# Kernel tuning notes

Measured on AMD Instinct MI355X. Metric: run time of the kernel, lower is better.

Reference implementation:

```python
import jax, jax.numpy as jnp
import numpy as np

B, D = 8192, 512
MARGIN, CR_BETA, NUM_CLASSES = 0.2, 0.1, 1000


def setup_inputs() -> dict:
    key = jax.random.key(0)
    k1, k2, k3, k4 = jax.random.split(key, 4)
    return {
        "img": jax.random.normal(k1, (B, D), jnp.float32),
        "txt": jax.random.normal(k2, (B, D), jnp.float32),
        "txt_cr": jax.random.normal(k3, (B, D), jnp.float32),
        "labels": jax.random.randint(k4, (B,), 0, NUM_CLASSES),
        "auto_margin_flag": 1,
        "margin": jnp.full((B,), MARGIN, jnp.float32),  # opt.margin repeated per row
        "cr_beta": CR_BETA,
    }


def _similarity(a, b):
    # row-normalize then full cosine-similarity matrix + matched (diagonal) sims
    an = a / (jnp.linalg.norm(a, axis=1, keepdims=True) + 1e-8)
    bn = b / (jnp.linalg.norm(b, axis=1, keepdims=True) + 1e-8)
    return an @ bn.T, jnp.sum(an * bn, axis=1)


def _dir_loss(sim, labels, margin, auto_flag):
    # semi-hard negative mining per anchor row, fully vectorized.
    # Deterministic stand-in for np.random.choice: first valid negative index.
    diag = jnp.diagonal(sim)                               # sim[idx, idx]
    neg_mask = labels[None, :] != labels[:, None]          # [B,B] negatives
    loss_mat = sim - diag[:, None] + margin[:, None]       # triplet margin term
    valid = neg_mask & (loss_mat > 0) & (loss_mat < margin[:, None])
    valid = jax.lax.stop_gradient(valid)                   # mining is detached (numpy in torch)
    has_valid = jnp.any(valid, axis=1)
    if auto_flag:
        row_ok = (margin >= 0.16) & has_valid
    else:
        row_ok = has_valid
    neg_idx = jnp.argmax(valid, axis=1)                    # first valid negative
    sim_an = jnp.take_along_axis(sim, neg_idx[:, None], axis=1)[:, 0]
    per_row = jax.nn.relu(margin - diag + sim_an)
    return jnp.sum(jnp.where(row_ok, per_row, 0.0))


def _cr_loss(img, txt, txt_cr, labels, auto_flag, margin, cr_beta):
    sim, sm = _similarity(img, txt)
    sim_cr, sm_cr = _similarity(img, txt_cr)
    if auto_flag:
        lam = jnp.abs(jax.lax.stop_gradient(sm_cr)) / jnp.abs(jax.lax.stop_gradient(sm))
        lam = jnp.minimum(lam, 1.0)                        # clamp lambda_cr to <= 1
        margin_cr = (lam + 1.0) * margin / 2.0
    else:
        margin_cr = margin / 2.0
    margin_cr = jax.lax.stop_gradient(margin_cr)
    base = _dir_loss(sim, labels, margin, auto_flag) + _dir_loss(sim.T, labels, margin, auto_flag)
    cr = _dir_loss(sim_cr, labels, margin_cr, auto_flag) + _dir_loss(sim_cr.T, labels, margin_cr, auto_flag)
    return base + cr_beta * cr


def reference(img, txt, txt_cr, labels, auto_margin_flag, margin, cr_beta):
    return _cr_loss(img, txt, txt_cr, labels, bool(auto_margin_flag), margin, cr_beta)
```

## Files before the change

### kernel.cpp

```cpp
#include <hip/hip_runtime.h>
#include <climits>

#define NB 8192
#define ND 512

#define WCHUNKS 16
#define WTILES 8
#define TCHUNKS ((NB - 64) / 64)


__global__ __launch_bounds__(256) void stats_k(
        const float* __restrict__ img, const float* __restrict__ txt,
        const float* __restrict__ cr, const float* __restrict__ margin,
        const int* __restrict__ flagp,
        float* rnImg, float* rnTxt, float* rnCr,
        float* dgSim, float* dgCr, float* mgCr,
        int* negIdx, int* stragCnt, float* out) {
    int tid = threadIdx.x, bid = blockIdx.x;
    int g = bid * 256 + tid;
    if (g < 4 * NB) negIdx[g] = INT_MAX;
    if (bid == 0 && tid < 8) stragCnt[tid] = 0;
    if (bid == 0 && tid == 0) out[0] = 0.0f;

    int r = bid * 16 + (tid >> 4);
    int q = tid & 15;
    const float4* iv = (const float4*)(img + (size_t)r * ND);
    const float4* tv = (const float4*)(txt + (size_t)r * ND);
    const float4* cv = (const float4*)(cr  + (size_t)r * ND);
    float sii = 0, stt = 0, scc = 0, sit = 0, sic = 0;
    #pragma unroll
    for (int i = 0; i < 8; ++i) {
        int k = q + i * 16;
        float4 x = iv[k], y = tv[k], w = cv[k];
        sii += x.x*x.x + x.y*x.y + x.z*x.z + x.w*x.w;
        stt += y.x*y.x + y.y*y.y + y.z*y.z + y.w*y.w;
        scc += w.x*w.x + w.y*w.y + w.z*w.z + w.w*w.w;
        sit += x.x*y.x + x.y*y.y + x.z*y.z + x.w*y.w;
        sic += x.x*w.x + x.y*w.y + x.z*w.z + x.w*w.w;
    }
    #pragma unroll
    for (int off = 1; off < 16; off <<= 1) {
        sii += __shfl_xor(sii, off); stt += __shfl_xor(stt, off);
        scc += __shfl_xor(scc, off); sit += __shfl_xor(sit, off);
        sic += __shfl_xor(sic, off);
    }
    if (q == 0) {
        float rnI = 1.0f / (sqrtf(sii) + 1e-8f);
        float rnT = 1.0f / (sqrtf(stt) + 1e-8f);
        float rnC = 1.0f / (sqrtf(scc) + 1e-8f);
        float ds = sit * rnI * rnT;
        float dc = sic * rnI * rnC;
        float m  = margin[r];
        float mcr = flagp[0] ? (fminf(fabsf(dc) / fabsf(ds), 1.0f) + 1.0f) * m * 0.5f
                             : m * 0.5f;
        rnImg[r] = rnI; rnTxt[r] = rnT; rnCr[r] = rnC;
        dgSim[r] = ds;  dgCr[r]  = dc;  mgCr[r] = mcr;
    }
}

__device__ inline void pass_arrays(int z,
        const float* img, const float* txt, const float* cr,
        const float* rnImg, const float* rnTxt, const float* rnCr,
        const float* dgSim, const float* dgCr,
        const float* margin, const float* mgCr,
        const float*& A, const float*& B, const float*& rnA, const float*& rnB,
        const float*& dgA, const float*& mgA) {
    if (z == 0)      { A = img; B = txt; rnA = rnImg; rnB = rnTxt; dgA = dgSim; mgA = margin; }
    else if (z == 1) { A = txt; B = img; rnA = rnTxt; rnB = rnImg; dgA = dgSim; mgA = margin; }
    else if (z == 2) { A = img; B = cr;  rnA = rnImg; rnB = rnCr;  dgA = dgCr;  mgA = mgCr;   }
    else             { A = cr;  B = img; rnA = rnCr;  rnB = rnImg; dgA = dgCr;  mgA = mgCr;   }
}

template <bool GATHER>
__device__ __forceinline__ void gemm32x64(
        const float* __restrict__ A, const float* __restrict__ B,
        int a0, const int* aRow, int c0,
        float (&As)[16][36], float (&Bs)[16][68],
        float (&acc)[2][4], int tid) {
    const int ty2 = (tid >> 4) * 2, tx4 = (tid & 15) * 4;
    const int lrow = tid >> 2, lk4 = (tid & 3) * 4;
    const bool doA = tid < 128;
    const int arow = GATHER ? (doA ? aRow[lrow] : 0) : (a0 + (lrow & 31));
    float4 va, vb;
    if (doA) va = *(const float4*)(A + (size_t)arow * ND + lk4);
    vb = *(const float4*)(B + (size_t)(c0 + lrow) * ND + lk4);
    for (int kc = 0; kc < ND; kc += 16) {
        __syncthreads();
        if (doA) {
            As[lk4 + 0][lrow] = va.x; As[lk4 + 1][lrow] = va.y;
            As[lk4 + 2][lrow] = va.z; As[lk4 + 3][lrow] = va.w;
        }
        Bs[lk4 + 0][lrow] = vb.x; Bs[lk4 + 1][lrow] = vb.y;
        Bs[lk4 + 2][lrow] = vb.z; Bs[lk4 + 3][lrow] = vb.w;
        if (kc + 16 < ND) {
            if (doA) va = *(const float4*)(A + (size_t)arow * ND + kc + 16 + lk4);
            vb = *(const float4*)(B + (size_t)(c0 + lrow) * ND + kc + 16 + lk4);
        }
        __syncthreads();
        #pragma unroll
        for (int k = 0; k < 16; ++k) {
            float2 av = *(const float2*)&As[k][ty2];
            float4 bv = *(const float4*)&Bs[k][tx4];
            #pragma unroll
            for (int i = 0; i < 2; ++i) {
                float ai = i ? av.y : av.x;
                acc[i][0] = fmaf(ai, bv.x, acc[i][0]);
                acc[i][1] = fmaf(ai, bv.y, acc[i][1]);
                acc[i][2] = fmaf(ai, bv.z, acc[i][2]);
                acc[i][3] = fmaf(ai, bv.w, acc[i][3]);
            }
        }
    }
}

__global__ __launch_bounds__(256) void band_k(
        const float* __restrict__ img, const float* __restrict__ txt,
        const float* __restrict__ cr, const int* __restrict__ labels,
        const int* __restrict__ flagp, const float* __restrict__ margin,
        const float* __restrict__ betap,
        const float* rnImg, const float* rnTxt, const float* rnCr,
        const float* dgSim, const float* dgCr, const float* mgCr,
        int* stragCnt, int* stragList, float* out) {
    __shared__ __align__(16) float As[16][36];
    __shared__ __align__(16) float Bs[16][68];
    __shared__ float aRn[32], aDg[32], aMg[32], colRn[64];
    __shared__ int   aLab[32], colLab[64], resIdx[32];
    __shared__ float blockAcc;

    const int tid = threadIdx.x, z = blockIdx.y, a0 = blockIdx.x * 32;
    const int flag = flagp[0];
    const float *A, *B, *rnA, *rnB, *dgA, *mgA;
    pass_arrays(z, img, txt, cr, rnImg, rnTxt, rnCr, dgSim, dgCr, margin, mgCr,
                A, B, rnA, rnB, dgA, mgA);

    if (tid < 32) {
        int a = a0 + tid;
        float mg = mgA[a];
        aRn[tid] = rnA[a]; aDg[tid] = dgA[a]; aMg[tid] = mg;
        aLab[tid] = labels[a];
        resIdx[tid] = (flag && mg < 0.16f) ? -1 : INT_MAX;
    }
    if (tid < 64) { colRn[tid] = rnB[tid]; colLab[tid] = labels[tid]; }
    if (tid == 0) blockAcc = 0.0f;
    __syncthreads();

    float acc[2][4] = {};
    gemm32x64<false>(A, B, a0, nullptr, 0, As, Bs, acc, tid);
    __syncthreads();

    const int ty2 = (tid >> 4) * 2, tx4 = (tid & 15) * 4;
    #pragma unroll
    for (int i = 0; i < 2; ++i) {
        int r = ty2 + i;
        float mgv = aMg[r];
        if (flag && mgv < 0.16f) continue;
        float dg = aDg[r], rna = aRn[r];
        int la = aLab[r];
        #pragma unroll
        for (int j = 0; j < 4; ++j) {
            int c = tx4 + j;
            if (colLab[c] == la) continue;
            float lm = acc[i][j] * rna * colRn[c] - dg + mgv;
            if (lm > 0.0f && lm < mgv) atomicMin(&resIdx[r], c);
        }
    }
    __syncthreads();

    #pragma unroll
    for (int i = 0; i < 2; ++i) {
        int r = ty2 + i;
        int w = resIdx[r];
        if (w < 0 || w == INT_MAX) continue;
        int c = w - tx4;
        if (c < 0 || c > 3) continue;
        float lm = acc[i][c] * aRn[r] * colRn[w] - aDg[r] + aMg[r];
        atomicAdd(&blockAcc, lm);
    }
    __syncthreads();

    if (tid < 32 && resIdx[tid] == INT_MAX) {
        int pos = atomicAdd(&stragCnt[z], 1);
        stragList[z * NB + pos] = a0 + tid;
    }
    if (tid == 0 && blockAcc != 0.0f) {
        float scale = (z >= 2) ? betap[0] : 1.0f;
        atomicAdd(out, blockAcc * scale);
    }
}

__global__ __launch_bounds__(256) void wina_k(
        const float* __restrict__ img, const float* __restrict__ txt,
        const float* __restrict__ cr, const int* __restrict__ labels,
        const float* __restrict__ margin,
        const float* rnImg, const float* rnTxt, const float* rnCr,
        const float* dgSim, const float* dgCr, const float* mgCr,
        const int* stragCnt, const int* stragList, int* negIdx) {
    __shared__ __align__(16) float As[16][36];
    __shared__ __align__(16) float Bs[16][68];
    __shared__ float aRn[32], aDg[32], aMg[32], colRn[64];
    __shared__ int   aId[32], aRow[32], aLab[32], colLab[64];

    const int tid = threadIdx.x, z = blockIdx.y;
    const int chunk = blockIdx.x & (WCHUNKS - 1);
    const int t     = blockIdx.x / WCHUNKS;
    const int cnt = stragCnt[z];
    if (t * 32 >= cnt) return;
    const int c0 = 64 + chunk * 64;

    const float *A, *B, *rnA, *rnB, *dgA, *mgA;
    pass_arrays(z, img, txt, cr, rnImg, rnTxt, rnCr, dgSim, dgCr, margin, mgCr,
                A, B, rnA, rnB, dgA, mgA);

    if (tid < 32) {
        int s = t * 32 + tid;
        int a = (s < cnt) ? stragList[z * NB + s] : -1;
        int ar = (a >= 0) ? a : 0;
        aId[tid] = a; aRow[tid] = ar;
        aRn[tid] = rnA[ar]; aDg[tid] = dgA[ar]; aMg[tid] = mgA[ar];
        aLab[tid] = labels[ar];
    }
    if (tid < 64) { colRn[tid] = rnB[c0 + tid]; colLab[tid] = labels[c0 + tid]; }
    __syncthreads();

    float acc[2][4] = {};
    gemm32x64<true>(A, B, 0, aRow, c0, As, Bs, acc, tid);
    __syncthreads();

    const int ty2 = (tid >> 4) * 2, tx4 = (tid & 15) * 4;
    #pragma unroll
    for (int i = 0; i < 2; ++i) {
        int r = ty2 + i;
        int a = aId[r];
        if (a < 0) continue;
        float dg = aDg[r], mgv = aMg[r], rna = aRn[r];
        int la = aLab[r];
        #pragma unroll
        for (int j = 0; j < 4; ++j) {
            int c = tx4 + j;
            if (colLab[c] == la) continue;
            float lm = acc[i][j] * rna * colRn[c] - dg + mgv;
            if (lm > 0.0f && lm < mgv) atomicMin(&negIdx[z * NB + a], c0 + c);
        }
    }
}

__device__ inline float dot8(const float4& a0, const float4& a1,
                             const float4& b0, const float4& b1) {
    return a0.x*b0.x + a0.y*b0.y + a0.z*b0.z + a0.w*b0.w
         + a1.x*b1.x + a1.y*b1.y + a1.z*b1.z + a1.w*b1.w;
}

__global__ __launch_bounds__(256) void tail_k(
        const float* __restrict__ img, const float* __restrict__ txt,
        const float* __restrict__ cr, const int* __restrict__ labels,
        const float* __restrict__ margin,
        const float* rnImg, const float* rnTxt, const float* rnCr,
        const float* dgSim, const float* dgCr, const float* mgCr,
        const int* stragCnt, const int* stragList, int* negIdx) {
    __shared__ __align__(16) float Aload[8][ND];
    __shared__ float sRn[8], sDg[8], sMg[8];
    __shared__ int   sLab[8], sAid[8];
    __shared__ float colRn_s[64];
    __shared__ int   colLab_s[64];
    __shared__ int   sSurv[256];
    __shared__ int   sNa;

    const int tid = threadIdx.x, z = blockIdx.y;
    const int c0 = 64 + blockIdx.x * 64;
    const int cnt = stragCnt[z];
    if (cnt == 0) return;

    const float *A, *B, *rnA, *rnB, *dgA, *mgA;
    pass_arrays(z, img, txt, cr, rnImg, rnTxt, rnCr, dgSim, dgCr, margin, mgCr,
                A, B, rnA, rnB, dgA, mgA);

    if (tid == 0) sNa = 0;
    __syncthreads();
    for (int s = tid; s < cnt; s += 256) {
        int a = stragList[z * NB + s];
        if (negIdx[z * NB + a] == INT_MAX) {
            int p = atomicAdd(&sNa, 1);
            if (p < 256) sSurv[p] = a;
        }
    }
    __syncthreads();
    const int na = min(sNa, 256);
    if (na == 0) return;

    if (tid < 64) { colRn_s[tid] = rnB[c0 + tid]; colLab_s[tid] = labels[c0 + tid]; }

    const int wv = tid >> 6, lane = tid & 63;

    for (int g0 = 0; g0 < na; g0 += 8) {
        const int gn = min(8, na - g0);
        __syncthreads();
        if (tid < 8) {
            int s = g0 + ((tid < gn) ? tid : 0);
            int a = sSurv[s];
            sAid[tid] = (tid < gn) ? a : -1;
            sRn[tid] = rnA[a]; sDg[tid] = dgA[a]; sMg[tid] = mgA[a];
            sLab[tid] = labels[a];
        }
        #pragma unroll
        for (int m = 0; m < 4; ++m) {
            int idx = tid + m * 256;
            int row = idx >> 7, f4 = idx & 127;
            int a = sSurv[g0 + ((row < gn) ? row : 0)];
            *(float4*)&Aload[row][f4 * 4] =
                *(const float4*)(A + (size_t)a * ND + f4 * 4);
        }
        __syncthreads();

        for (int cb = 0; cb < 16; cb += 4) {
            const int cc0 = wv * 16 + cb;
            float4 b0[4], b1[4];
            #pragma unroll
            for (int q = 0; q < 4; ++q) {
                const float4* Bv = (const float4*)(B + (size_t)(c0 + cc0 + q) * ND);
                b0[q] = Bv[lane]; b1[q] = Bv[lane + 64];
            }
            #pragma unroll
            for (int s = 0; s < 8; ++s) {
                float4 a0v = *(const float4*)&Aload[s][lane * 4];
                float4 a1v = *(const float4*)&Aload[s][(lane + 64) * 4];
                float d0 = dot8(a0v, a1v, b0[0], b1[0]);
                float d1 = dot8(a0v, a1v, b0[1], b1[1]);
                float d2 = dot8(a0v, a1v, b0[2], b1[2]);
                float d3 = dot8(a0v, a1v, b0[3], b1[3]);
                #pragma unroll
                for (int off = 1; off < 64; off <<= 1) {
                    d0 += __shfl_xor(d0, off); d1 += __shfl_xor(d1, off);
                    d2 += __shfl_xor(d2, off); d3 += __shfl_xor(d3, off);
                }
                if (lane == 0) {
                    int aid = sAid[s];
                    if (aid >= 0) {
                        float rn = sRn[s], dg = sDg[s], mg = sMg[s];
                        int lb = sLab[s];
                        float dv[4] = {d0, d1, d2, d3};
                        #pragma unroll
                        for (int q = 0; q < 4; ++q) {
                            int cc = cc0 + q;
                            if (colLab_s[cc] != lb) {
                                float lm = dv[q] * rn * colRn_s[cc] - dg + mg;
                                if (lm > 0.0f && lm < mg)
                                    atomicMin(&negIdx[z * NB + aid], c0 + cc);
                            }
                        }
                    }
                }
            }
        }
    }
}

__global__ __launch_bounds__(256) void final_k(
        const float* __restrict__ img, const float* __restrict__ txt,
        const float* __restrict__ cr,
        const float* rnImg, const float* rnTxt, const float* rnCr,
        const float* dgSim, const float* dgCr,
        const float* __restrict__ margin, const float* mgCr,
        const float* __restrict__ betap,
        const int* stragCnt, const int* stragList, const int* negIdx,
        float* out) {
    __shared__ float s4[4];
    const int tid = threadIdx.x, z = blockIdx.y;
    const float *A, *B, *rnA, *rnB, *dgA, *mgA;
    pass_arrays(z, img, txt, cr, rnImg, rnTxt, rnCr, dgSim, dgCr, margin, mgCr,
                A, B, rnA, rnB, dgA, mgA);
    int t = blockIdx.x * 256 + tid;
    float contrib = 0.0f;
    if (t < stragCnt[z]) {
        int a = stragList[z * NB + t];
        int idx = negIdx[z * NB + a];
        if (idx != INT_MAX) {
            const float4* Av = (const float4*)(A + (size_t)a   * ND);
            const float4* Bv = (const float4*)(B + (size_t)idx * ND);
            float d = 0.0f;
            #pragma unroll 8
            for (int i = 0; i < ND / 4; ++i) {
                float4 x = Av[i], y = Bv[i];
                d += x.x*y.x + x.y*y.y + x.z*y.z + x.w*y.w;
            }
            float lm = d * rnA[a] * rnB[idx] - dgA[a] + mgA[a];
            contrib = fmaxf(lm, 0.0f);
        }
    }
    #pragma unroll
    for (int off = 32; off; off >>= 1) contrib += __shfl_xor(contrib, off);
    if ((tid & 63) == 0) s4[tid >> 6] = contrib;
    __syncthreads();
    if (tid == 0) {
        float sum = s4[0] + s4[1] + s4[2] + s4[3];
        if (sum != 0.0f) atomicAdd(out, sum * ((z >= 2) ? betap[0] : 1.0f));
    }
}


__global__ __launch_bounds__(256) void zero_k(float* out, int n) {
    int g = blockIdx.x * 256 + threadIdx.x;
    if (g < n) out[g] = 0.0f;
}

template <int U>
__device__ void stragScan(const float* __restrict__ A, const float* __restrict__ B,
                          const int* __restrict__ labels, int a0, int u, int scol,
                          const int* sList, int g0,
                          const float* aRn, const float* aDg, const float* aMg,
                          const int* aLab, int* sMin8, int* doneMask,
                          float* blockAcc) {
    const int tid = threadIdx.x;
    float rn_s[U], dg_s[U], mg_s[U];
    int lab_s[U];
    const float4* Av[U];
    #pragma unroll
    for (int s = 0; s < U; ++s) {
        int slot = sList[g0 + (s < u ? s : 0)];
        rn_s[s] = aRn[slot]; dg_s[s] = aDg[slot]; mg_s[s] = aMg[slot];
        lab_s[s] = aLab[slot];
        Av[s] = (const float4*)(A + (size_t)(a0 + slot) * ND);
    }
    if (tid < U) sMin8[tid] = INT_MAX;
    if (tid == 0) *doneMask = 0;
    __syncthreads();
    for (int jb = scol; jb < NB; jb += 256) {
        int j = jb + tid;
        bool jv = (j < NB);
        int mask = *doneMask;
        float dot[U];
        #pragma unroll
        for (int s = 0; s < U; ++s) dot[s] = 0.0f;
        float ssq = 0.0f;
        if (jv) {
            const float4* Bv = (const float4*)(B + (size_t)j * ND);
            #pragma unroll 4
            for (int k4 = 0; k4 < ND / 4; ++k4) {
                float4 b = Bv[k4];
                ssq += b.x*b.x + b.y*b.y + b.z*b.z + b.w*b.w;
                #pragma unroll
                for (int s = 0; s < U; ++s) {
                    float4 a = Av[s][k4];
                    dot[s] += a.x*b.x + a.y*b.y + a.z*b.z + a.w*b.w;
                }
            }
        }
        float rnb = 1.0f / (sqrtf(ssq) + 1e-8f);
        int lj = jv ? labels[j] : -1;
        float lmv[U];
        #pragma unroll
        for (int s = 0; s < U; ++s) {
            lmv[s] = dot[s] * rn_s[s] * rnb - dg_s[s] + mg_s[s];
            if (jv && s < u && !((mask >> s) & 1) && lj != lab_s[s] &&
                lmv[s] > 0.0f && lmv[s] < mg_s[s])
                atomicMin(&sMin8[s], j);
        }
        __syncthreads();
        #pragma unroll
        for (int s = 0; s < U; ++s)
            if (jv && s < u && !((mask >> s) & 1) && sMin8[s] == j)
                atomicAdd(blockAcc, lmv[s]);
        __syncthreads();
        if (tid == 0) {
            int m2 = 0;
            for (int s = 0; s < u; ++s)
                if (sMin8[s] != INT_MAX) m2 |= (1 << s);
            *doneMask = m2;
        }
        __syncthreads();
        if (*doneMask == (1 << u) - 1) break;
    }
}

__global__ __launch_bounds__(256) void mine_k(const float* __restrict__ img,
                                              const float* __restrict__ txt,
                                              const float* __restrict__ cr,
                                              const int*   __restrict__ labels,
                                              const int*   __restrict__ flagp,
                                              const float* __restrict__ margin,
                                              const float* __restrict__ betap,
                                              float* __restrict__ out) {
    __shared__ __align__(16) float As[16][64];
    __shared__ __align__(16) float Bs[16][64];
    __shared__ float aRn[64], aDg[64], aMg[64];
    __shared__ int   aLab[64];
    __shared__ float colRn[64];
    __shared__ int   colLab[64];
    __shared__ int   resIdx[64], prevIdx[64];
    __shared__ int   cnt;
    __shared__ float blockAcc;
    __shared__ int   sList[64];
    __shared__ int   sCnt;
    __shared__ int   sMin8[8];
    __shared__ int   doneMask;

    const int tid  = threadIdx.x;
    const int z    = blockIdx.y;
    const int a0   = blockIdx.x * 64;
    const int flag = flagp[0];
    const float* A = (z == 1) ? txt : (z == 3) ? cr : img;
    const float* B = (z == 0) ? txt : (z == 2) ? cr : img;
    {
        int ar = tid >> 2, q = tid & 3;
        int a  = a0 + ar;
        const float4* iv = (const float4*)(img + (size_t)a * ND) + q * 32;
        const float4* tv = (const float4*)(txt + (size_t)a * ND) + q * 32;
        const float4* cv = (const float4*)(cr  + (size_t)a * ND) + q * 32;
        float sii = 0, stt = 0, scc = 0, sit = 0, sic = 0;
        #pragma unroll 4
        for (int i = 0; i < 32; ++i) {
            float4 x = iv[i], y = tv[i], w = cv[i];
            sii += x.x*x.x + x.y*x.y + x.z*x.z + x.w*x.w;
            stt += y.x*y.x + y.y*y.y + y.z*y.z + y.w*y.w;
            scc += w.x*w.x + w.y*w.y + w.z*w.z + w.w*w.w;
            sit += x.x*y.x + x.y*y.y + x.z*y.z + x.w*y.w;
            sic += x.x*w.x + x.y*w.y + x.z*w.z + x.w*w.w;
        }
        sii += __shfl_xor(sii, 1); sii += __shfl_xor(sii, 2);
        stt += __shfl_xor(stt, 1); stt += __shfl_xor(stt, 2);
        sit += __shfl_xor(sit, 1); sit += __shfl_xor(sit, 2);
        scc += __shfl_xor(scc, 1); scc += __shfl_xor(scc, 2);
        sic += __shfl_xor(sic, 1); sic += __shfl_xor(sic, 2);
        if (q == 0) {
            float rnI = 1.0f / (sqrtf(sii) + 1e-8f);
            float rnT = 1.0f / (sqrtf(stt) + 1e-8f);
            float ds  = sit * rnI * rnT;
            float m   = margin[a];
            float mg, rna, dgv;
            if (z >= 2) {
                float rnC = 1.0f / (sqrtf(scc) + 1e-8f);
                float dc  = sic * rnI * rnC;
                mg = flag ? (fminf(fabsf(dc) / fabsf(ds), 1.0f) + 1.0f) * m * 0.5f
                          : m * 0.5f;
                dgv = dc; rna = (z == 3) ? rnC : rnI;
            } else {
                mg = m; dgv = ds; rna = (z == 1) ? rnT : rnI;
            }
            aRn[ar] = rna; aDg[ar] = dgv; aMg[ar] = mg; aLab[ar] = labels[a];
            resIdx[ar] = (flag && mg < 0.16f) ? -1 : INT_MAX;
        }
        if (tid == 0) blockAcc = 0.0f;
    }
    __syncthreads();
    const int ty4  = (tid >> 4) * 4, tx4 = (tid & 15) * 4;
    const int lrow = tid >> 2,  lk4 = (tid & 3) * 4;
    int bandCols = 0, unresolved = 64;
    for (int jc = 0; jc < 2; ++jc) {
        int j0 = jc * 64;
        float acc[4][4];
        #pragma unroll
        for (int i = 0; i < 4; ++i)
            #pragma unroll
            for (int j = 0; j < 4; ++j) acc[i][j] = 0.0f;
        float bssq = 0.0f;
        for (int kc = 0; kc < ND; kc += 16) {
            __syncthreads();
            float4 va = *(const float4*)(A + (size_t)(a0 + lrow) * ND + kc + lk4);
            float4 vb = *(const float4*)(B + (size_t)(j0 + lrow) * ND + kc + lk4);
            As[lk4 + 0][lrow] = va.x; As[lk4 + 1][lrow] = va.y;
            As[lk4 + 2][lrow] = va.z; As[lk4 + 3][lrow] = va.w;
            Bs[lk4 + 0][lrow] = vb.x; Bs[lk4 + 1][lrow] = vb.y;
            Bs[lk4 + 2][lrow] = vb.z; Bs[lk4 + 3][lrow] = vb.w;
            bssq += vb.x*vb.x + vb.y*vb.y + vb.z*vb.z + vb.w*vb.w;
            __syncthreads();
            #pragma unroll
            for (int k = 0; k < 16; ++k) {
                float4 av = *(const float4*)&As[k][ty4];
                float4 bv = *(const float4*)&Bs[k][tx4];
                float ar[4] = {av.x, av.y, av.z, av.w};
                float br[4] = {bv.x, bv.y, bv.z, bv.w};
                #pragma unroll
                for (int i = 0; i < 4; ++i)
                    #pragma unroll
                    for (int j = 0; j < 4; ++j)
                        acc[i][j] = fmaf(ar[i], br[j], acc[i][j]);
            }
        }
        bssq += __shfl_xor(bssq, 1); bssq += __shfl_xor(bssq, 2);
        __syncthreads();
        if ((tid & 3) == 0) {
            colRn[lrow]  = 1.0f / (sqrtf(bssq) + 1e-8f);
            colLab[lrow] = labels[j0 + lrow];
        }
        if (tid < 64) prevIdx[tid] = resIdx[tid];
        __syncthreads();
        #pragma unroll
        for (int i = 0; i < 4; ++i) {
            int r = ty4 + i;
            if (prevIdx[r] != INT_MAX) continue;
            float dg = aDg[r], mgv = aMg[r], rna = aRn[r];
            int la = aLab[r];
            #pragma unroll
            for (int j = 0; j < 4; ++j) {
                int c = tx4 + j;
                if (colLab[c] == la) continue;
                float v  = acc[i][j] * rna * colRn[c];
                float lm = v - dg + mgv;
                if (lm > 0.0f && lm < mgv) atomicMin(&resIdx[r], j0 + c);
            }
        }
        __syncthreads();
        #pragma unroll
        for (int i = 0; i < 4; ++i) {
            int r = ty4 + i;
            if (prevIdx[r] != INT_MAX) continue;
            int w = resIdx[r];
            if (w == INT_MAX) continue;
            int c = w - j0 - tx4;
            if (c < 0 || c > 3) continue;
            float v  = acc[i][c] * aRn[r] * colRn[tx4 + c];
            float lm = v - aDg[r] + aMg[r];
            atomicAdd(&blockAcc, lm);
        }
        __syncthreads();
        if (tid == 0) cnt = 0;
        __syncthreads();
        if (tid < 64 && resIdx[tid] == INT_MAX) atomicAdd(&cnt, 1);
        __syncthreads();
        unresolved = cnt;
        bandCols = j0 + 64;
        __syncthreads();
        if (unresolved <= 8) break;
    }
    if (unresolved > 0) {
        if (tid == 0) sCnt = 0;
        __syncthreads();
        if (tid < 64 && resIdx[tid] == INT_MAX) {
            int pos = atomicAdd(&sCnt, 1);
            sList[pos] = tid;
        }
        __syncthreads();
        int total = sCnt;
        for (int g0 = 0; g0 < total; g0 += 8) {
            int u = min(8, total - g0);
            if (u == 1)      stragScan<1>(A, B, labels, a0, u, bandCols, sList, g0, aRn, aDg, aMg, aLab, sMin8, &doneMask, &blockAcc);
            else if (u == 2) stragScan<2>(A, B, labels, a0, u, bandCols, sList, g0, aRn, aDg, aMg, aLab, sMin8, &doneMask, &blockAcc);
            else if (u <= 4) stragScan<4>(A, B, labels, a0, u, bandCols, sList, g0, aRn, aDg, aMg, aLab, sMin8, &doneMask, &blockAcc);
            else             stragScan<8>(A, B, labels, a0, u, bandCols, sList, g0, aRn, aDg, aMg, aLab, sMin8, &doneMask, &blockAcc);
            __syncthreads();
        }
    }
    if (tid == 0 && blockAcc != 0.0f) {
        float scale = (z >= 2) ? betap[0] : 1.0f;
        atomicAdd(out, blockAcc * scale);
    }
}


extern "C" void kernel_launch(void* const* d_in, const int* in_sizes, int n_in,
                              void* d_out, int out_size, void* d_ws, size_t ws_size,
                              hipStream_t stream) {
    const float* img    = (const float*)d_in[0];
    const float* txt    = (const float*)d_in[1];
    const float* cr     = (const float*)d_in[2];
    const int*   labels = (const int*)  d_in[3];
    const int*   flagp  = (const int*)  d_in[4];
    const float* marg   = (const float*)d_in[5];
    const float* betap  = (const float*)d_in[6];
    float* out = (float*)d_out;
    (void)in_sizes; (void)n_in;

    const size_t REQ = (size_t)(6 * NB) * 4 + (size_t)(4 * NB) * 4 + 64 +
                       (size_t)(4 * NB) * 4;
    if (ws_size >= REQ) {
        float* wf = (float*)d_ws;
        float* rnImg = wf + 0 * NB;
        float* rnTxt = wf + 1 * NB;
        float* rnCr  = wf + 2 * NB;
        float* dgSim = wf + 3 * NB;
        float* dgCr  = wf + 4 * NB;
        float* mgCr  = wf + 5 * NB;
        int* negIdx    = (int*)(wf + 6 * NB);
        int* stragCnt  = negIdx + 4 * NB;
        int* stragList = stragCnt + 16;

        stats_k<<<dim3(NB / 16),              dim3(256), 0, stream>>>(
            img, txt, cr, marg, flagp,
            rnImg, rnTxt, rnCr, dgSim, dgCr, mgCr, negIdx, stragCnt, out);
        band_k <<<dim3(NB / 32, 4),           dim3(256), 0, stream>>>(
            img, txt, cr, labels, flagp, marg, betap,
            rnImg, rnTxt, rnCr, dgSim, dgCr, mgCr, stragCnt, stragList, out);
        wina_k <<<dim3(WCHUNKS * WTILES, 4),  dim3(256), 0, stream>>>(
            img, txt, cr, labels, marg,
            rnImg, rnTxt, rnCr, dgSim, dgCr, mgCr,
            stragCnt, stragList, negIdx);
        tail_k <<<dim3(TCHUNKS, 4),           dim3(256), 0, stream>>>(
            img, txt, cr, labels, marg,
            rnImg, rnTxt, rnCr, dgSim, dgCr, mgCr,
            stragCnt, stragList, negIdx);
        final_k<<<dim3(NB / 256, 4),          dim3(256), 0, stream>>>(
            img, txt, cr, rnImg, rnTxt, rnCr, dgSim, dgCr, marg, mgCr, betap,
            stragCnt, stragList, negIdx, out);
    } else {
        zero_k<<<dim3((out_size + 255) / 256), dim3(256), 0, stream>>>(out, out_size);
        mine_k<<<dim3(NB / 64, 4), dim3(256), 0, stream>>>(img, txt, cr, labels,
                                                           flagp, marg, betap, out);
    }
}
```

Before: 242.1 us.

## Fuse band passes sharing img tile and shrink tail chunk width

Replaces the four-pass band kernel with a two-pass kernel. Each block computes 64x64 tiles for both the base and cross-reference similarities, sharing one img tile across both GEMMs, so img loads are halved and each thread gets a larger 4x4 register tile. The tail kernel now uses 32-column chunks, which doubles the grid. It skips chunks already covered by the window kernel when the straggler count is small, and loops only over valid gathered rows. The costs are higher register pressure from two 4x4 accumulators per thread and more tail blocks, each reloading anchor rows.

After: 227.1 us. 6.2% less time.

```diff
diff --git a/kernel.cpp b/kernel.cpp
--- a/kernel.cpp
+++ b/kernel.cpp
@@ -6,7 +6,7 @@
 
 #define WCHUNKS 16
 #define WTILES 8
-#define TCHUNKS ((NB - 64) / 64)
+#define TCHUNKS ((NB - 64) / 32)
 
 
 __global__ __launch_bounds__(256) void stats_k(
@@ -71,13 +71,200 @@
     else             { A = cr;  B = img; rnA = rnCr;  rnB = rnImg; dgA = dgCr;  mgA = mgCr;   }
 }
 
+__global__ __launch_bounds__(256) void band2_k(
+        const float* __restrict__ img, const float* __restrict__ txt,
+        const float* __restrict__ cr, const int* __restrict__ labels,
+        const int* __restrict__ flagp, const float* __restrict__ margin,
+        const float* __restrict__ betap,
+        const float* rnImg, const float* rnTxt, const float* rnCr,
+        const float* dgSim, const float* dgCr, const float* mgCr,
+        int* stragCnt, int* stragList, float* out) {
+    __shared__ __align__(16) float T0[16][68];
+    __shared__ __align__(16) float T1[16][68];
+    __shared__ __align__(16) float T2[16][68];
+    __shared__ float aRn1[64], aDg1[64], aMg1[64];
+    __shared__ float aRn2[64], aDg2[64], aMg2[64];
+    __shared__ float cRn1[64], cRn2[64];
+    __shared__ int   aLab[64], cLab[64], res1[64], res2[64];
+    __shared__ float bAcc1, bAcc2;
+
+    const int tid = threadIdx.x, pair = blockIdx.y, a0 = blockIdx.x * 64;
+    const int flag = flagp[0];
+
+    if (tid < 64) {
+        int a = a0 + tid;
+        aLab[tid] = labels[a];
+        cLab[tid] = labels[tid];
+        float m = margin[a], mc = mgCr[a];
+        if (pair == 0) {
+            float rn = rnImg[a];
+            aRn1[tid] = rn;         aDg1[tid] = dgSim[a]; aMg1[tid] = m;
+            aRn2[tid] = rn;         aDg2[tid] = dgCr[a];  aMg2[tid] = mc;
+            cRn1[tid] = rnTxt[tid]; cRn2[tid] = rnCr[tid];
+        } else {
+            aRn1[tid] = rnTxt[a];   aDg1[tid] = dgSim[a]; aMg1[tid] = m;
+            aRn2[tid] = rnCr[a];    aDg2[tid] = dgCr[a];  aMg2[tid] = mc;
+            float ri = rnImg[tid];  cRn1[tid] = ri;       cRn2[tid] = ri;
+        }
+        res1[tid] = (flag && m  < 0.16f) ? -1 : INT_MAX;
+        res2[tid] = (flag && mc < 0.16f) ? -1 : INT_MAX;
+    }
+    if (tid == 0) { bAcc1 = 0.0f; bAcc2 = 0.0f; }
+
+    const int lrow = tid >> 2, lk4 = (tid & 3) * 4;
+    const int rImg = pair ? lrow : (a0 + lrow);
+    const int rTC  = pair ? (a0 + lrow) : lrow;
+    const float* p0 = img + (size_t)rImg * ND + lk4;
+    const float* p1 = txt + (size_t)rTC  * ND + lk4;
+    const float* p2 = cr  + (size_t)rTC  * ND + lk4;
+
+    const int ty4 = (tid >> 4) * 4, tx4 = (tid & 15) * 4;
+    float acc1[4][4] = {}, acc2[4][4] = {};
+
+    float4 v0 = *(const float4*)p0;
+    float4 v1 = *(const float4*)p1;
+    float4 v2 = *(const float4*)p2;
+
+    if (pair == 0) {
+        for (int kc = 0; kc < ND; kc += 16) {
+            __syncthreads();
+            T0[lk4 + 0][lrow] = v0.x; T0[lk4 + 1][lrow] = v0.y;
+            T0[lk4 + 2][lrow] = v0.z; T0[lk4 + 3][lrow] = v0.w;
+            T1[lk4 + 0][lrow] = v1.x; T1[lk4 + 1][lrow] = v1.y;
+            T1[lk4 + 2][lrow] = v1.z; T1[lk4 + 3][lrow] = v1.w;
+            T2[lk4 + 0][lrow] = v2.x; T2[lk4 + 1][lrow] = v2.y;
+            T2[lk4 + 2][lrow] = v2.z; T2[lk4 + 3][lrow] = v2.w;
+            if (kc + 16 < ND) {
+                v0 = *(const float4*)(p0 + kc + 16);
+                v1 = *(const float4*)(p1 + kc + 16);
+                v2 = *(const float4*)(p2 + kc + 16);
+            }
+            __syncthreads();
+            #pragma unroll
+            for (int k = 0; k < 16; ++k) {
+                float4 rv = *(const float4*)&T0[k][ty4];
+                float4 c1 = *(const float4*)&T1[k][tx4];
+                float4 c2 = *(const float4*)&T2[k][tx4];
+                float rr[4] = {rv.x, rv.y, rv.z, rv.w};
+                float b1[4] = {c1.x, c1.y, c1.z, c1.w};
+                float b2[4] = {c2.x, c2.y, c2.z, c2.w};
+                #pragma unroll
+                for (int i = 0; i < 4; ++i)
+                    #pragma unroll
+                    for (int j = 0; j < 4; ++j) {
+                        acc1[i][j] = fmaf(rr[i], b1[j], acc1[i][j]);
+                        acc2[i][j] = fmaf(rr[i], b2[j], acc2[i][j]);
+                    }
+            }
+        }
+    } else {
+        for (int kc = 0; kc < ND; kc += 16) {
+            __syncthreads();
+            T0[lk4 + 0][lrow] = v0.x; T0[lk4 + 1][lrow] = v0.y;
+            T0[lk4 + 2][lrow] = v0.z; T0[lk4 + 3][lrow] = v0.w;
+            T1[lk4 + 0][lrow] = v1.x; T1[lk4 + 1][lrow] = v1.y;
+            T1[lk4 + 2][lrow] = v1.z; T1[lk4 + 3][lrow] = v1.w;
+            T2[lk4 + 0][lrow] = v2.x; T2[lk4 + 1][lrow] = v2.y;
+            T2[lk4 + 2][lrow] = v2.z; T2[lk4 + 3][lrow] = v2.w;
+            if (kc + 16 < ND) {
+                v0 = *(const float4*)(p0 + kc + 16);
+                v1 = *(const float4*)(p1 + kc + 16);
+                v2 = *(const float4*)(p2 + kc + 16);
+            }
+            __syncthreads();
+            #pragma unroll
+            for (int k = 0; k < 16; ++k) {
+                float4 r1 = *(const float4*)&T1[k][ty4];
+                float4 r2 = *(const float4*)&T2[k][ty4];
+                float4 cv = *(const float4*)&T0[k][tx4];
+                float a1[4] = {r1.x, r1.y, r1.z, r1.w};
+                float a2[4] = {r2.x, r2.y, r2.z, r2.w};
+                float bb[4] = {cv.x, cv.y, cv.z, cv.w};
+                #pragma unroll
+                for (int i = 0; i < 4; ++i)
+                    #pragma unroll
+                    for (int j = 0; j < 4; ++j) {
+                        acc1[i][j] = fmaf(a1[i], bb[j], acc1[i][j]);
+                        acc2[i][j] = fmaf(a2[i], bb[j], acc2[i][j]);
+                    }
+            }
+        }
+    }
+    __syncthreads();
+
+    #pragma unroll
+    for (int i = 0; i < 4; ++i) {
+        int r = ty4 + i;
+        int la = aLab[r];
+        float mg1 = aMg1[r];
+        if (!(flag && mg1 < 0.16f)) {
+            float dg = aDg1[r], rn = aRn1[r];
+            #pragma unroll
+            for (int j = 0; j < 4; ++j) {
+                int c = tx4 + j;
+                if (cLab[c] == la) continue;
+                float lm = acc1[i][j] * rn * cRn1[c] - dg + mg1;
+                if (lm > 0.0f && lm < mg1) atomicMin(&res1[r], c);
+            }
+        }
+        float mg2 = aMg2[r];
+        if (!(flag && mg2 < 0.16f)) {
+            float dg = aDg2[r], rn = aRn2[r];
+            #pragma unroll
+            for (int j = 0; j < 4; ++j) {
+                int c = tx4 + j;
+                if (cLab[c] == la) continue;
+                float lm = acc2[i][j] * rn * cRn2[c] - dg + mg2;
+                if (lm > 0.0f && lm < mg2) atomicMin(&res2[r], c);
+            }
+        }
+    }
+    __syncthreads();
+
+    #pragma unroll
+    for (int i = 0; i < 4; ++i) {
+        int r = ty4 + i;
+        int w = res1[r];
+        if (w >= 0 && w != INT_MAX) {
+            int c = w - tx4;
+            if (c >= 0 && c <= 3) {
+                float lm = acc1[i][c] * aRn1[r] * cRn1[w] - aDg1[r] + aMg1[r];
+                atomicAdd(&bAcc1, lm);
+            }
+        }
+        int w2 = res2[r];
+        if (w2 >= 0 && w2 != INT_MAX) {
+            int c = w2 - tx4;
+            if (c >= 0 && c <= 3) {
+                float lm = acc2[i][c] * aRn2[r] * cRn2[w2] - aDg2[r] + aMg2[r];
+                atomicAdd(&bAcc2, lm);
+            }
+        }
+    }
+    __syncthreads();
+
+    if (tid < 64) {
+        if (res1[tid] == INT_MAX) {
+            int pos = atomicAdd(&stragCnt[pair], 1);
+            stragList[pair * NB + pos] = a0 + tid;
+        }
+        if (res2[tid] == INT_MAX) {
+            int pos = atomicAdd(&stragCnt[pair + 2], 1);
+            stragList[(pair + 2) * NB + pos] = a0 + tid;
+        }
+    }
+    if (tid == 0) {
+        float t = bAcc1 + betap[0] * bAcc2;
+        if (t != 0.0f) atomicAdd(out, t);
+    }
+}
+
 template <bool GATHER>
 __device__ __forceinline__ void gemm32x64(
         const float* __restrict__ A, const float* __restrict__ B,
         int a0, const int* aRow, int c0,
         float (&As)[16][36], float (&Bs)[16][68],
         float (&acc)[2][4], int tid) {
-    const int ty2 = (tid >> 4) * 2, tx4 = (tid & 15) * 4;
     const int lrow = tid >> 2, lk4 = (tid & 3) * 4;
     const bool doA = tid < 128;
     const int arow = GATHER ? (doA ? aRow[lrow] : 0) : (a0 + (lrow & 31));
@@ -97,6 +284,7 @@
             vb = *(const float4*)(B + (size_t)(c0 + lrow) * ND + kc + 16 + lk4);
         }
         __syncthreads();
+        const int ty2 = (tid >> 4) * 2, tx4 = (tid & 15) * 4;
         #pragma unroll
         for (int k = 0; k < 16; ++k) {
             float2 av = *(const float2*)&As[k][ty2];
@@ -110,81 +298,6 @@
                 acc[i][3] = fmaf(ai, bv.w, acc[i][3]);
             }
         }
-    }
-}
-
-__global__ __launch_bounds__(256) void band_k(
-        const float* __restrict__ img, const float* __restrict__ txt,
-        const float* __restrict__ cr, const int* __restrict__ labels,
-        const int* __restrict__ flagp, const float* __restrict__ margin,
-        const float* __restrict__ betap,
-        const float* rnImg, const float* rnTxt, const float* rnCr,
-        const float* dgSim, const float* dgCr, const float* mgCr,
-        int* stragCnt, int* stragList, float* out) {
-    __shared__ __align__(16) float As[16][36];
-    __shared__ __align__(16) float Bs[16][68];
-    __shared__ float aRn[32], aDg[32], aMg[32], colRn[64];
-    __shared__ int   aLab[32], colLab[64], resIdx[32];
-    __shared__ float blockAcc;
-
-    const int tid = threadIdx.x, z = blockIdx.y, a0 = blockIdx.x * 32;
-    const int flag = flagp[0];
-    const float *A, *B, *rnA, *rnB, *dgA, *mgA;
-    pass_arrays(z, img, txt, cr, rnImg, rnTxt, rnCr, dgSim, dgCr, margin, mgCr,
-                A, B, rnA, rnB, dgA, mgA);
-
-    if (tid < 32) {
-        int a = a0 + tid;
-        float mg = mgA[a];
-        aRn[tid] = rnA[a]; aDg[tid] = dgA[a]; aMg[tid] = mg;
-        aLab[tid] = labels[a];
-        resIdx[tid] = (flag && mg < 0.16f) ? -1 : INT_MAX;
-    }
-    if (tid < 64) { colRn[tid] = rnB[tid]; colLab[tid] = labels[tid]; }
-    if (tid == 0) blockAcc = 0.0f;
-    __syncthreads();
-
-    float acc[2][4] = {};
-    gemm32x64<false>(A, B, a0, nullptr, 0, As, Bs, acc, tid);
-    __syncthreads();
-
-    const int ty2 = (tid >> 4) * 2, tx4 = (tid & 15) * 4;
-    #pragma unroll
-    for (int i = 0; i < 2; ++i) {
-        int r = ty2 + i;
-        float mgv = aMg[r];
-        if (flag && mgv < 0.16f) continue;
-        float dg = aDg[r], rna = aRn[r];
-        int la = aLab[r];
-        #pragma unroll
-        for (int j = 0; j < 4; ++j) {
-            int c = tx4 + j;
-            if (colLab[c] == la) continue;
-            float lm = acc[i][j] * rna * colRn[c] - dg + mgv;
-            if (lm > 0.0f && lm < mgv) atomicMin(&resIdx[r], c);
-        }
-    }
-    __syncthreads();
-
-    #pragma unroll
-    for (int i = 0; i < 2; ++i) {
-        int r = ty2 + i;
-        int w = resIdx[r];
-        if (w < 0 || w == INT_MAX) continue;
-        int c = w - tx4;
-        if (c < 0 || c > 3) continue;
-        float lm = acc[i][c] * aRn[r] * colRn[w] - aDg[r] + aMg[r];
-        atomicAdd(&blockAcc, lm);
-    }
-    __syncthreads();
-
-    if (tid < 32 && resIdx[tid] == INT_MAX) {
-        int pos = atomicAdd(&stragCnt[z], 1);
-        stragList[z * NB + pos] = a0 + tid;
-    }
-    if (tid == 0 && blockAcc != 0.0f) {
-        float scale = (z >= 2) ? betap[0] : 1.0f;
-        atomicAdd(out, blockAcc * scale);
     }
 }
 
@@ -260,15 +373,16 @@
     __shared__ __align__(16) float Aload[8][ND];
     __shared__ float sRn[8], sDg[8], sMg[8];
     __shared__ int   sLab[8], sAid[8];
-    __shared__ float colRn_s[64];
-    __shared__ int   colLab_s[64];
+    __shared__ float colRn_s[32];
+    __shared__ int   colLab_s[32];
     __shared__ int   sSurv[256];
     __shared__ int   sNa;
 
     const int tid = threadIdx.x, z = blockIdx.y;
-    const int c0 = 64 + blockIdx.x * 64;
+    const int c0 = 64 + blockIdx.x * 32;
     const int cnt = stragCnt[z];
     if (cnt == 0) return;
+    if (cnt <= WTILES * 32 && c0 < 64 + WCHUNKS * 64) return;
 
     const float *A, *B, *rnA, *rnB, *dgA, *mgA;
     pass_arrays(z, img, txt, cr, rnImg, rnTxt, rnCr, dgSim, dgCr, margin, mgCr,
@@ -287,7 +401,7 @@
     const int na = min(sNa, 256);
     if (na == 0) return;
 
-    if (tid < 64) { colRn_s[tid] = rnB[c0 + tid]; colLab_s[tid] = labels[c0 + tid]; }
+    if (tid < 32) { colRn_s[tid] = rnB[c0 + tid]; colLab_s[tid] = labels[c0 + tid]; }
 
     const int wv = tid >> 6, lane = tid & 63;
 
@@ -305,22 +419,24 @@
         for (int m = 0; m < 4; ++m) {
             int idx = tid + m * 256;
             int row = idx >> 7, f4 = idx & 127;
-            int a = sSurv[g0 + ((row < gn) ? row : 0)];
-            *(float4*)&Aload[row][f4 * 4] =
-                *(const float4*)(A + (size_t)a * ND + f4 * 4);
-        }
-        __syncthreads();
-
-        for (int cb = 0; cb < 16; cb += 4) {
-            const int cc0 = wv * 16 + cb;
+            if (row < gn) {
+                int a = sSurv[g0 + row];
+                *(float4*)&Aload[row][f4 * 4] =
+                    *(const float4*)(A + (size_t)a * ND + f4 * 4);
+            }
+        }
+        __syncthreads();
+
+        #pragma unroll
+        for (int cb = 0; cb < 2; ++cb) {
+            const int cc0 = wv * 8 + cb * 4;
             float4 b0[4], b1[4];
             #pragma unroll
             for (int q = 0; q < 4; ++q) {
                 const float4* Bv = (const float4*)(B + (size_t)(c0 + cc0 + q) * ND);
                 b0[q] = Bv[lane]; b1[q] = Bv[lane + 64];
             }
-            #pragma unroll
-            for (int s = 0; s < 8; ++s) {
+            for (int s = 0; s < gn; ++s) {
                 float4 a0v = *(const float4*)&Aload[s][lane * 4];
                 float4 a1v = *(const float4*)&Aload[s][(lane + 64) * 4];
                 float d0 = dot8(a0v, a1v, b0[0], b1[0]);
@@ -334,18 +450,16 @@
                 }
                 if (lane == 0) {
                     int aid = sAid[s];
-                    if (aid >= 0) {
-                        float rn = sRn[s], dg = sDg[s], mg = sMg[s];
-                        int lb = sLab[s];
-                        float dv[4] = {d0, d1, d2, d3};
-                        #pragma unroll
-                        for (int q = 0; q < 4; ++q) {
-                            int cc = cc0 + q;
-                            if (colLab_s[cc] != lb) {
-                                float lm = dv[q] * rn * colRn_s[cc] - dg + mg;
-                                if (lm > 0.0f && lm < mg)
-                                    atomicMin(&negIdx[z * NB + aid], c0 + cc);
-                            }
+                    float rn = sRn[s], dg = sDg[s], mg = sMg[s];
+                    int lb = sLab[s];
+                    float dv[4] = {d0, d1, d2, d3};
+                    #pragma unroll
+                    for (int q = 0; q < 4; ++q) {
+                        int cc = cc0 + q;
+                        if (colLab_s[cc] != lb) {
+                            float lm = dv[q] * rn * colRn_s[cc] - dg + mg;
+                            if (lm > 0.0f && lm < mg)
+                                atomicMin(&negIdx[z * NB + aid], c0 + cc);
                         }
                     }
                 }
@@ -676,7 +790,7 @@
         stats_k<<<dim3(NB / 16),              dim3(256), 0, stream>>>(
             img, txt, cr, marg, flagp,
             rnImg, rnTxt, rnCr, dgSim, dgCr, mgCr, negIdx, stragCnt, out);
-        band_k <<<dim3(NB / 32, 4),           dim3(256), 0, stream>>>(
+        band2_k<<<dim3(NB / 64, 2),           dim3(256), 0, stream>>>(
             img, txt, cr, labels, flagp, marg, betap,
             rnImg, rnTxt, rnCr, dgSim, dgCr, mgCr, stragCnt, stragList, out);
         wina_k <<<dim3(WCHUNKS * WTILES, 4),  dim3(256), 0, stream>>>(
```

## Retile band and window GEMMs, narrow tail chunks, skip window-covered tail columns

Applied to the files above, without the earlier changes.

band_k now handles 64 anchor rows per block with a 4x4 per-thread micro-tile instead of 32 rows with 2x4. wina_k moves to 64-row by 32-column tiles spread over more column chunks. tail_k uses 32-column chunks and returns early when the window kernel already covered those columns for a small straggler count. The inner loop now runs only over the valid rows. The aim is more reuse per loaded tile, fewer wasted gathers, and less redundant tail scanning, at the cost of more registers and fewer band blocks.

After: 219.5 us. 9.3% less time.

```diff
diff --git a/kernel.cpp b/kernel.cpp
--- a/kernel.cpp
+++ b/kernel.cpp
@@ -4,9 +4,11 @@
 #define NB 8192
 #define ND 512
 
-#define WCHUNKS 16
-#define WTILES 8
-#define TCHUNKS ((NB - 64) / 64)
+#define WCHUNKS 32
+#define WTILES 4
+#define WCAP (WTILES * 64)
+#define WCOLS (64 + WCHUNKS * 32)
+#define TCHUNKS ((NB - 64) / 32)
 
 
 __global__ __launch_bounds__(256) void stats_k(
@@ -71,48 +73,6 @@
     else             { A = cr;  B = img; rnA = rnCr;  rnB = rnImg; dgA = dgCr;  mgA = mgCr;   }
 }
 
-template <bool GATHER>
-__device__ __forceinline__ void gemm32x64(
-        const float* __restrict__ A, const float* __restrict__ B,
-        int a0, const int* aRow, int c0,
-        float (&As)[16][36], float (&Bs)[16][68],
-        float (&acc)[2][4], int tid) {
-    const int ty2 = (tid >> 4) * 2, tx4 = (tid & 15) * 4;
-    const int lrow = tid >> 2, lk4 = (tid & 3) * 4;
-    const bool doA = tid < 128;
-    const int arow = GATHER ? (doA ? aRow[lrow] : 0) : (a0 + (lrow & 31));
-    float4 va, vb;
-    if (doA) va = *(const float4*)(A + (size_t)arow * ND + lk4);
-    vb = *(const float4*)(B + (size_t)(c0 + lrow) * ND + lk4);
-    for (int kc = 0; kc < ND; kc += 16) {
-        __syncthreads();
-        if (doA) {
-            As[lk4 + 0][lrow] = va.x; As[lk4 + 1][lrow] = va.y;
-            As[lk4 + 2][lrow] = va.z; As[lk4 + 3][lrow] = va.w;
-        }
-        Bs[lk4 + 0][lrow] = vb.x; Bs[lk4 + 1][lrow] = vb.y;
-        Bs[lk4 + 2][lrow] = vb.z; Bs[lk4 + 3][lrow] = vb.w;
-        if (kc + 16 < ND) {
-            if (doA) va = *(const float4*)(A + (size_t)arow * ND + kc + 16 + lk4);
-            vb = *(const float4*)(B + (size_t)(c0 + lrow) * ND + kc + 16 + lk4);
-        }
-        __syncthreads();
-        #pragma unroll
-        for (int k = 0; k < 16; ++k) {
-            float2 av = *(const float2*)&As[k][ty2];
-            float4 bv = *(const float4*)&Bs[k][tx4];
-            #pragma unroll
-            for (int i = 0; i < 2; ++i) {
-                float ai = i ? av.y : av.x;
-                acc[i][0] = fmaf(ai, bv.x, acc[i][0]);
-                acc[i][1] = fmaf(ai, bv.y, acc[i][1]);
-                acc[i][2] = fmaf(ai, bv.z, acc[i][2]);
-                acc[i][3] = fmaf(ai, bv.w, acc[i][3]);
-            }
-        }
-    }
-}
-
 __global__ __launch_bounds__(256) void band_k(
         const float* __restrict__ img, const float* __restrict__ txt,
         const float* __restrict__ cr, const int* __restrict__ labels,
@@ -121,37 +81,68 @@
         const float* rnImg, const float* rnTxt, const float* rnCr,
         const float* dgSim, const float* dgCr, const float* mgCr,
         int* stragCnt, int* stragList, float* out) {
-    __shared__ __align__(16) float As[16][36];
+    __shared__ __align__(16) float As[16][68];
     __shared__ __align__(16) float Bs[16][68];
-    __shared__ float aRn[32], aDg[32], aMg[32], colRn[64];
-    __shared__ int   aLab[32], colLab[64], resIdx[32];
+    __shared__ float aRn[64], aDg[64], aMg[64], colRn[64];
+    __shared__ int   aLab[64], colLab[64], resIdx[64];
     __shared__ float blockAcc;
 
-    const int tid = threadIdx.x, z = blockIdx.y, a0 = blockIdx.x * 32;
+    const int tid = threadIdx.x, z = blockIdx.y, a0 = blockIdx.x * 64;
     const int flag = flagp[0];
     const float *A, *B, *rnA, *rnB, *dgA, *mgA;
     pass_arrays(z, img, txt, cr, rnImg, rnTxt, rnCr, dgSim, dgCr, margin, mgCr,
                 A, B, rnA, rnB, dgA, mgA);
 
-    if (tid < 32) {
+    if (tid < 64) {
         int a = a0 + tid;
         float mg = mgA[a];
         aRn[tid] = rnA[a]; aDg[tid] = dgA[a]; aMg[tid] = mg;
         aLab[tid] = labels[a];
+        colRn[tid] = rnB[tid]; colLab[tid] = labels[tid];
         resIdx[tid] = (flag && mg < 0.16f) ? -1 : INT_MAX;
     }
-    if (tid < 64) { colRn[tid] = rnB[tid]; colLab[tid] = labels[tid]; }
     if (tid == 0) blockAcc = 0.0f;
-    __syncthreads();
-
-    float acc[2][4] = {};
-    gemm32x64<false>(A, B, a0, nullptr, 0, As, Bs, acc, tid);
-    __syncthreads();
-
-    const int ty2 = (tid >> 4) * 2, tx4 = (tid & 15) * 4;
-    #pragma unroll
-    for (int i = 0; i < 2; ++i) {
-        int r = ty2 + i;
+
+    const int ty4  = (tid >> 4) * 4, tx4 = (tid & 15) * 4;
+    const int lrow = tid >> 2,  lk4 = (tid & 3) * 4;
+
+    float acc[4][4];
+    #pragma unroll
+    for (int i = 0; i < 4; ++i)
+        #pragma unroll
+        for (int j = 0; j < 4; ++j) acc[i][j] = 0.0f;
+
+    float4 va = *(const float4*)(A + (size_t)(a0 + lrow) * ND + lk4);
+    float4 vb = *(const float4*)(B + (size_t)lrow * ND + lk4);
+    for (int kc = 0; kc < ND; kc += 16) {
+        __syncthreads();
+        As[lk4 + 0][lrow] = va.x; As[lk4 + 1][lrow] = va.y;
+        As[lk4 + 2][lrow] = va.z; As[lk4 + 3][lrow] = va.w;
+        Bs[lk4 + 0][lrow] = vb.x; Bs[lk4 + 1][lrow] = vb.y;
+        Bs[lk4 + 2][lrow] = vb.z; Bs[lk4 + 3][lrow] = vb.w;
+        if (kc + 16 < ND) {
+            va = *(const float4*)(A + (size_t)(a0 + lrow) * ND + kc + 16 + lk4);
+            vb = *(const float4*)(B + (size_t)lrow * ND + kc + 16 + lk4);
+        }
+        __syncthreads();
+        #pragma unroll
+        for (int k = 0; k < 16; ++k) {
+            float4 av = *(const float4*)&As[k][ty4];
+            float4 bv = *(const float4*)&Bs[k][tx4];
+            float ar[4] = {av.x, av.y, av.z, av.w};
+            float br[4] = {bv.x, bv.y, bv.z, bv.w};
+            #pragma unroll
+            for (int i = 0; i < 4; ++i)
+                #pragma unroll
+                for (int j = 0; j < 4; ++j)
+                    acc[i][j] = fmaf(ar[i], br[j], acc[i][j]);
+        }
+    }
+    __syncthreads();
+
+    #pragma unroll
+    for (int i = 0; i < 4; ++i) {
+        int r = ty4 + i;
         float mgv = aMg[r];
         if (flag && mgv < 0.16f) continue;
         float dg = aDg[r], rna = aRn[r];
@@ -167,8 +158,8 @@
     __syncthreads();
 
     #pragma unroll
-    for (int i = 0; i < 2; ++i) {
-        int r = ty2 + i;
+    for (int i = 0; i < 4; ++i) {
+        int r = ty4 + i;
         int w = resIdx[r];
         if (w < 0 || w == INT_MAX) continue;
         int c = w - tx4;
@@ -178,7 +169,7 @@
     }
     __syncthreads();
 
-    if (tid < 32 && resIdx[tid] == INT_MAX) {
+    if (tid < 64 && resIdx[tid] == INT_MAX) {
         int pos = atomicAdd(&stragCnt[z], 1);
         stragList[z * NB + pos] = a0 + tid;
     }
@@ -195,48 +186,82 @@
         const float* rnImg, const float* rnTxt, const float* rnCr,
         const float* dgSim, const float* dgCr, const float* mgCr,
         const int* stragCnt, const int* stragList, int* negIdx) {
-    __shared__ __align__(16) float As[16][36];
-    __shared__ __align__(16) float Bs[16][68];
-    __shared__ float aRn[32], aDg[32], aMg[32], colRn[64];
-    __shared__ int   aId[32], aRow[32], aLab[32], colLab[64];
+    __shared__ __align__(16) float As[16][68];
+    __shared__ __align__(16) float Bs[16][36];
+    __shared__ float aRn[64], aDg[64], aMg[64], colRn[32];
+    __shared__ int   aId[64], aRow[64], aLab[64], colLab[32];
 
     const int tid = threadIdx.x, z = blockIdx.y;
     const int chunk = blockIdx.x & (WCHUNKS - 1);
     const int t     = blockIdx.x / WCHUNKS;
     const int cnt = stragCnt[z];
-    if (t * 32 >= cnt) return;
-    const int c0 = 64 + chunk * 64;
+    if (t * 64 >= cnt) return;
+    const int c0 = 64 + chunk * 32;
 
     const float *A, *B, *rnA, *rnB, *dgA, *mgA;
     pass_arrays(z, img, txt, cr, rnImg, rnTxt, rnCr, dgSim, dgCr, margin, mgCr,
                 A, B, rnA, rnB, dgA, mgA);
 
-    if (tid < 32) {
-        int s = t * 32 + tid;
+    if (tid < 64) {
+        int s = t * 64 + tid;
         int a = (s < cnt) ? stragList[z * NB + s] : -1;
         int ar = (a >= 0) ? a : 0;
         aId[tid] = a; aRow[tid] = ar;
         aRn[tid] = rnA[ar]; aDg[tid] = dgA[ar]; aMg[tid] = mgA[ar];
         aLab[tid] = labels[ar];
     }
-    if (tid < 64) { colRn[tid] = rnB[c0 + tid]; colLab[tid] = labels[c0 + tid]; }
-    __syncthreads();
-
-    float acc[2][4] = {};
-    gemm32x64<true>(A, B, 0, aRow, c0, As, Bs, acc, tid);
-    __syncthreads();
-
-    const int ty2 = (tid >> 4) * 2, tx4 = (tid & 15) * 4;
-    #pragma unroll
-    for (int i = 0; i < 2; ++i) {
-        int r = ty2 + i;
+    if (tid < 32) { colRn[tid] = rnB[c0 + tid]; colLab[tid] = labels[c0 + tid]; }
+    __syncthreads();
+
+    const int ty4  = (tid >> 4) * 4, tx2 = (tid & 15) * 2;
+    const int lrow = tid >> 2,  lk4 = (tid & 3) * 4;
+    const int arow = aRow[lrow];
+    const bool doB = tid < 128;
+
+    float acc[4][2];
+    #pragma unroll
+    for (int i = 0; i < 4; ++i) { acc[i][0] = 0.0f; acc[i][1] = 0.0f; }
+
+    float4 va = *(const float4*)(A + (size_t)arow * ND + lk4);
+    float4 vb;
+    if (doB) vb = *(const float4*)(B + (size_t)(c0 + lrow) * ND + lk4);
+    for (int kc = 0; kc < ND; kc += 16) {
+        __syncthreads();
+        As[lk4 + 0][lrow] = va.x; As[lk4 + 1][lrow] = va.y;
+        As[lk4 + 2][lrow] = va.z; As[lk4 + 3][lrow] = va.w;
+        if (doB) {
+            Bs[lk4 + 0][lrow] = vb.x; Bs[lk4 + 1][lrow] = vb.y;
+            Bs[lk4 + 2][lrow] = vb.z; Bs[lk4 + 3][lrow] = vb.w;
+        }
+        if (kc + 16 < ND) {
+            va = *(const float4*)(A + (size_t)arow * ND + kc + 16 + lk4);
+            if (doB) vb = *(const float4*)(B + (size_t)(c0 + lrow) * ND + kc + 16 + lk4);
+        }
+        __syncthreads();
+        #pragma unroll
+        for (int k = 0; k < 16; ++k) {
+            float4 av = *(const float4*)&As[k][ty4];
+            float2 bv = *(const float2*)&Bs[k][tx2];
+            float ar[4] = {av.x, av.y, av.z, av.w};
+            #pragma unroll
+            for (int i = 0; i < 4; ++i) {
+                acc[i][0] = fmaf(ar[i], bv.x, acc[i][0]);
+                acc[i][1] = fmaf(ar[i], bv.y, acc[i][1]);
+            }
+        }
+    }
+    __syncthreads();
+
+    #pragma unroll
+    for (int i = 0; i < 4; ++i) {
+        int r = ty4 + i;
         int a = aId[r];
         if (a < 0) continue;
         float dg = aDg[r], mgv = aMg[r], rna = aRn[r];
         int la = aLab[r];
         #pragma unroll
-        for (int j = 0; j < 4; ++j) {
-            int c = tx4 + j;
+        for (int j = 0; j < 2; ++j) {
+            int c = tx2 + j;
             if (colLab[c] == la) continue;
             float lm = acc[i][j] * rna * colRn[c] - dg + mgv;
             if (lm > 0.0f && lm < mgv) atomicMin(&negIdx[z * NB + a], c0 + c);
@@ -260,15 +285,16 @@
     __shared__ __align__(16) float Aload[8][ND];
     __shared__ float sRn[8], sDg[8], sMg[8];
     __shared__ int   sLab[8], sAid[8];
-    __shared__ float colRn_s[64];
-    __shared__ int   colLab_s[64];
+    __shared__ float colRn_s[32];
+    __shared__ int   colLab_s[32];
     __shared__ int   sSurv[256];
     __shared__ int   sNa;
 
     const int tid = threadIdx.x, z = blockIdx.y;
-    const int c0 = 64 + blockIdx.x * 64;
+    const int c0 = 64 + blockIdx.x * 32;
     const int cnt = stragCnt[z];
     if (cnt == 0) return;
+    if (cnt <= WCAP && c0 < WCOLS) return;
 
     const float *A, *B, *rnA, *rnB, *dgA, *mgA;
     pass_arrays(z, img, txt, cr, rnImg, rnTxt, rnCr, dgSim, dgCr, margin, mgCr,
@@ -287,7 +313,7 @@
     const int na = min(sNa, 256);
     if (na == 0) return;
 
-    if (tid < 64) { colRn_s[tid] = rnB[c0 + tid]; colLab_s[tid] = labels[c0 + tid]; }
+    if (tid < 32) { colRn_s[tid] = rnB[c0 + tid]; colLab_s[tid] = labels[c0 + tid]; }
 
     const int wv = tid >> 6, lane = tid & 63;
 
@@ -305,22 +331,24 @@
         for (int m = 0; m < 4; ++m) {
             int idx = tid + m * 256;
             int row = idx >> 7, f4 = idx & 127;
-            int a = sSurv[g0 + ((row < gn) ? row : 0)];
-            *(float4*)&Aload[row][f4 * 4] =
-                *(const float4*)(A + (size_t)a * ND + f4 * 4);
-        }
-        __syncthreads();
-
-        for (int cb = 0; cb < 16; cb += 4) {
-            const int cc0 = wv * 16 + cb;
+            if (row < gn) {
+                int a = sSurv[g0 + row];
+                *(float4*)&Aload[row][f4 * 4] =
+                    *(const float4*)(A + (size_t)a * ND + f4 * 4);
+            }
+        }
+        __syncthreads();
+
+        #pragma unroll
+        for (int cb = 0; cb < 2; ++cb) {
+            const int cc0 = wv * 8 + cb * 4;
             float4 b0[4], b1[4];
             #pragma unroll
             for (int q = 0; q < 4; ++q) {
                 const float4* Bv = (const float4*)(B + (size_t)(c0 + cc0 + q) * ND);
                 b0[q] = Bv[lane]; b1[q] = Bv[lane + 64];
             }
-            #pragma unroll
-            for (int s = 0; s < 8; ++s) {
+            for (int s = 0; s < gn; ++s) {
                 float4 a0v = *(const float4*)&Aload[s][lane * 4];
                 float4 a1v = *(const float4*)&Aload[s][(lane + 64) * 4];
                 float d0 = dot8(a0v, a1v, b0[0], b1[0]);
@@ -334,18 +362,16 @@
                 }
                 if (lane == 0) {
                     int aid = sAid[s];
-                    if (aid >= 0) {
-                        float rn = sRn[s], dg = sDg[s], mg = sMg[s];
-                        int lb = sLab[s];
-                        float dv[4] = {d0, d1, d2, d3};
-                        #pragma unroll
-                        for (int q = 0; q < 4; ++q) {
-                            int cc = cc0 + q;
-                            if (colLab_s[cc] != lb) {
-                                float lm = dv[q] * rn * colRn_s[cc] - dg + mg;
-                                if (lm > 0.0f && lm < mg)
-                                    atomicMin(&negIdx[z * NB + aid], c0 + cc);
-                            }
+                    float rn = sRn[s], dg = sDg[s], mg = sMg[s];
+                    int lb = sLab[s];
+                    float dv[4] = {d0, d1, d2, d3};
+                    #pragma unroll
+                    for (int q = 0; q < 4; ++q) {
+                        int cc = cc0 + q;
+                        if (colLab_s[cc] != lb) {
+                            float lm = dv[q] * rn * colRn_s[cc] - dg + mg;
+                            if (lm > 0.0f && lm < mg)
+                                atomicMin(&negIdx[z * NB + aid], c0 + cc);
                         }
                     }
                 }
@@ -676,7 +702,7 @@
         stats_k<<<dim3(NB / 16),              dim3(256), 0, stream>>>(
             img, txt, cr, marg, flagp,
             rnImg, rnTxt, rnCr, dgSim, dgCr, mgCr, negIdx, stragCnt, out);
-        band_k <<<dim3(NB / 32, 4),           dim3(256), 0, stream>>>(
+        band_k <<<dim3(NB / 64, 4),           dim3(256), 0, stream>>>(
             img, txt, cr, labels, flagp, marg, betap,
             rnImg, rnTxt, rnCr, dgSim, dgCr, mgCr, stragCnt, stragList, out);
         wina_k <<<dim3(WCHUNKS * WTILES, 4),  dim3(256), 0, stream>>>(
```
